# Kernel optimization log

Hardware: AMD Instinct MI355X
Metric: run time of the kernel (lower is better)

## Reference

```python
import jax, jax.numpy as jnp
import numpy as np

NUM_BINS_X = 1024
NUM_BINS_Y = 1024
XL, XH, YL, YH = 0.0, 1024.0, 0.0, 1024.0
NUM_NODES = 4_000_000
NUM_FILLER = 1_000_000
NUM_PHYS = NUM_NODES - NUM_FILLER      # physical = movable + fixed
NUM_MOVABLE = 2_500_000
UNIT_PIN_CAPACITY = 2.0                # pins per unit area capacity
PIN_STRETCH_RATIO = 1.414              # DREAMPlace default sqrt(2)
MAX_ADJ = 2.5
MIN_ADJ = 1.0 / MAX_ADJ
SPAN = 4                               # max bins any box spans per axis (sizes <= 2*bin)


def setup_inputs() -> dict:
    key = jax.random.key(0)
    k1, k2, k3, k4, k5 = jax.random.split(key, 5)
    node_size_x = 0.5 + 1.5 * jax.random.uniform(k1, (NUM_NODES,), jnp.float32)
    node_size_y = 0.5 + 1.5 * jax.random.uniform(k2, (NUM_NODES,), jnp.float32)
    pos_x = XL + jax.random.uniform(k3, (NUM_NODES,), jnp.float32) * (XH - XL - 2.0)
    pos_y = YL + jax.random.uniform(k4, (NUM_NODES,), jnp.float32) * (YH - YL - 2.0)
    pos = jnp.concatenate([pos_x, pos_y])  # [2*num_nodes], x then y
    pin_weights = jax.random.randint(k5, (NUM_PHYS,), 1, 9, jnp.int32)
    return {"pos": pos, "node_size_x": node_size_x, "node_size_y": node_size_y,
            "pin_weights": pin_weights}


def _overlap(lo, hi, bin_lo, bin_size):
    # overlap length of interval [lo,hi] with bin [bin_lo, bin_lo+bin_size]
    return jnp.clip(jnp.minimum(hi, bin_lo + bin_size) - jnp.maximum(lo, bin_lo), 0.0, None)


def reference(pos, node_size_x, node_size_y, pin_weights):
    bsx = (XH - XL) / NUM_BINS_X
    bsy = (YH - YL) / NUM_BINS_Y
    dtype = pos.dtype

    # ---- phase 1: pin density map over stretched boxes of physical nodes ----
    sx = node_size_x[:NUM_PHYS]
    sy = node_size_y[:NUM_PHYS]
    hx = 0.5 * jnp.maximum(bsx * PIN_STRETCH_RATIO, sx)  # half stretched extent
    hy = 0.5 * jnp.maximum(bsy * PIN_STRETCH_RATIO, sy)
    cx = pos[:NUM_PHYS] + 0.5 * sx
    cy = pos[NUM_NODES:NUM_NODES + NUM_PHYS] + 0.5 * sy
    xmin, xmax = cx - hx, cx + hx
    ymin, ymax = cy - hy, cy + hy
    dens = pin_weights.astype(dtype) / (4.0 * hx * hy)   # pins per unit area

    bxl = jnp.clip(jnp.floor((xmin - XL) / bsx).astype(jnp.int32), 0, NUM_BINS_X - 1)
    byl = jnp.clip(jnp.floor((ymin - YL) / bsy).astype(jnp.int32), 0, NUM_BINS_Y - 1)

    pmap = jnp.zeros(NUM_BINS_X * NUM_BINS_Y, dtype)
    for di in range(SPAN):
        bx = bxl + di
        ox = _overlap(xmin, xmax, XL + bx.astype(dtype) * bsx, bsx)
        vx = bx < NUM_BINS_X
        for dj in range(SPAN):
            by = byl + dj
            oy = _overlap(ymin, ymax, YL + by.astype(dtype) * bsy, bsy)
            v = vx & (by < NUM_BINS_Y)
            idx = jnp.where(v, bx * NUM_BINS_Y + by, 0)
            val = jnp.where(v, dens * ox * oy, 0.0)
            pmap = pmap.at[idx].add(val)

    # density -> utilization: scatter added pins*overlap/area, divide by bin area
    pmap = pmap / (bsx * bsy)
    adj = jnp.clip(pmap / UNIT_PIN_CAPACITY, MIN_ADJ, MAX_ADJ)

    # ---- phase 2: per-movable-node pin-optimized area over actual footprint ----
    mx = pos[:NUM_MOVABLE]
    my = pos[NUM_NODES:NUM_NODES + NUM_MOVABLE]
    msx = node_size_x[:NUM_MOVABLE]
    msy = node_size_y[:NUM_MOVABLE]
    bxl2 = jnp.clip(jnp.floor((mx - XL) / bsx).astype(jnp.int32), 0, NUM_BINS_X - 1)
    byl2 = jnp.clip(jnp.floor((my - YL) / bsy).astype(jnp.int32), 0, NUM_BINS_Y - 1)

    area = jnp.zeros(NUM_MOVABLE, dtype)
    for di in range(SPAN):
        bx = bxl2 + di
        ox = _overlap(mx, mx + msx, XL + bx.astype(dtype) * bsx, bsx)
        vx = bx < NUM_BINS_X
        for dj in range(SPAN):
            by = byl2 + dj
            oy = _overlap(my, my + msy, YL + by.astype(dtype) * bsy, bsy)
            v = vx & (by < NUM_BINS_Y)
            idx = jnp.where(v, bx * NUM_BINS_Y + by, 0)
            area = area + jnp.where(v, ox * oy * adj[idx], 0.0)
    return area
```

## Files before the change

### kernel.cpp

```cpp
#include <hip/hip_runtime.h>

#define NBX 1024
#define NBY 1024
#define TS 64
#define NTX (NBX / TS)
#define NTY (NBY / TS)
#define NTILES (NTX * NTY)
#define LW 66
#define LSTRIDE 67
#define CAP 13056
#define CAPM 11008

#define FB_BLOCK 512
#define FB_K 4
#define FB_CHUNK (FB_BLOCK * FB_K)

#define PMAP_SCALE 131072.0f
#define PMAP_INV   (1.0f / 131072.0f)

static constexpr int NUM_NODES   = 4000000;
static constexpr int NUM_PHYS    = 3000000;
static constexpr int NUM_MOVABLE = 2500000;
static constexpr int HALF_MOV    = NUM_MOVABLE / 2;

typedef unsigned long long u64;

static constexpr size_t OFF_PMAP  = 0;
static constexpr size_t OFF_CURS  = OFF_PMAP + (size_t)NBX * NBY * 4;
static constexpr size_t OFF_CURSM = OFF_CURS + NTILES * 4;
static constexpr size_t OFF_SLAB  = ((OFF_CURSM + NTILES * 4 + 15) / 16) * 16;
static constexpr size_t OFF_MSLAB = ((OFF_SLAB + (size_t)NTILES * CAP * 8 + 15) / 16) * 16;
static constexpr size_t WS_FULL   = OFF_MSLAB + (size_t)NTILES * CAPM * 12;

__global__ void __launch_bounds__(FB_BLOCK)
fill_both(const float* __restrict__ pos, const float* __restrict__ nsx,
          const float* __restrict__ nsy, const int* __restrict__ pw,
          unsigned* __restrict__ curs, unsigned* __restrict__ cursm,
          uint2* __restrict__ slab, uint3* __restrict__ mslab) {
    __shared__ unsigned cntp[NTILES], cntm[NTILES];
    __shared__ unsigned offp[NTILES], offm[NTILES];
    __shared__ unsigned basep[NTILES], basem[NTILES];
    __shared__ unsigned wsum[8];
    __shared__ uint2 SAB[FB_CHUNK];
    __shared__ unsigned SC[FB_CHUNK];
    __shared__ unsigned short ST[FB_CHUNK];

    const int tid = threadIdx.x;
    const int b0  = blockIdx.x * FB_CHUNK;

    if (tid < NTILES) { cntp[tid] = 0u; cntm[tid] = 0u; }
    __syncthreads();

    u64 P[FB_K];
    u64 M[FB_K];
    int TPM[FB_K];
    unsigned rkP[FB_K], rkM[FB_K];

    #pragma unroll
    for (int k = 0; k < FB_K; ++k) {
        int i = b0 + k * FB_BLOCK + tid;
        int tp = -1, tm = -1;
        if (i < NUM_PHYS) {
            float mx = pos[i], my = pos[NUM_NODES + i];
            float sx = nsx[i], sy = nsy[i];
            float hx = 0.5f * fmaxf(1.414f, sx);
            float hy = 0.5f * fmaxf(1.414f, sy);
            unsigned qhx = (unsigned)__float2int_rn((hx - 0.7f) * 1024.0f);
            unsigned qhy = (unsigned)__float2int_rn((hy - 0.7f) * 1024.0f);
            float hxd = 0.7f + (float)qhx * (1.0f / 1024.0f);
            float hyd = 0.7f + (float)qhy * (1.0f / 1024.0f);
            float xmin = mx + 0.5f * sx - hxd;
            float ymin = my + 0.5f * sy - hyd;
            int bxl = min(max((int)floorf(xmin), 0), NBX - 1);
            int byl = min(max((int)floorf(ymin), 0), NBY - 1);
            tp = (bxl >> 6) * NTY + (byl >> 6);
            int bx0 = (tp >> 4) << 6, by0 = (tp & 15) << 6;
            unsigned ex = (unsigned)__float2int_rn((xmin - (float)bx0 + 1.0f) * 8192.0f);
            unsigned ey = (unsigned)__float2int_rn((ymin - (float)by0 + 1.0f) * 8192.0f);
            P[k] = (u64)ex | ((u64)ey << 20) | ((u64)qhx << 40)
                 | ((u64)qhy << 50) | ((u64)(unsigned)(pw[i] - 1) << 60);
            rkP[k] = atomicAdd(&cntp[tp], 1u);
            if (i < NUM_MOVABLE) {
                int bxm = min(max((int)floorf(mx), 0), NBX - 1);
                int bym = min(max((int)floorf(my), 0), NBY - 1);
                tm = (bxm >> 6) * NTY + (bym >> 6);
                int bx0m = (tm >> 4) << 6, by0m = (tm & 15) << 6;
                unsigned exm = (unsigned)__float2int_rn((mx - (float)bx0m) * 8192.0f);
                unsigned eym = (unsigned)__float2int_rn((my - (float)by0m) * 8192.0f);
                unsigned qsx = (unsigned)__float2int_rn((sx - 0.5f) * 2048.0f);
                unsigned qsy = (unsigned)__float2int_rn((sy - 0.5f) * 2048.0f);
                M[k] = (u64)exm | ((u64)eym << 20) | ((u64)qsx << 40) | ((u64)qsy << 52);
                rkM[k] = atomicAdd(&cntm[tm], 1u);
            }
        }
        TPM[k] = (tp & 0xffff) | (tm << 16);
    }
    __syncthreads();

    {
        const int lane   = tid & 63;
        const int scanId = tid & 255;
        const bool isMov = tid >= 256;
        unsigned* cnt = isMov ? cntm : cntp;
        unsigned* off = isMov ? offm : offp;
        unsigned* bs  = isMov ? basem : basep;
        unsigned* gc  = isMov ? cursm : curs;

        unsigned v = cnt[scanId];
        unsigned x = v;
        #pragma unroll
        for (int d = 1; d < 64; d <<= 1) {
            unsigned y = __shfl_up(x, d);
            if (lane >= d) x += y;
        }
        if (lane == 63) wsum[tid >> 6] = x;
        __syncthreads();
        unsigned add = 0;
        const int w0  = isMov ? 4 : 0;
        const int myw = scanId >> 6;
        for (int w = 0; w < myw; ++w) add += wsum[w0 + w];
        off[scanId] = x + add - v;
        bs[scanId]  = v ? atomicAdd(&gc[scanId], v) : 0u;
    }
    __syncthreads();

    #pragma unroll
    for (int k = 0; k < FB_K; ++k) {
        int tp = (int)(short)(TPM[k] & 0xffff);
        if (tp >= 0) {
            unsigned s = offp[tp] + rkP[k];
            SAB[s] = make_uint2((unsigned)P[k], (unsigned)(P[k] >> 32));
            ST[s]  = (unsigned short)tp;
        }
    }
    __syncthreads();

    {
        unsigned totP = offp[NTILES - 1] + cntp[NTILES - 1];
        for (unsigned j = tid; j < totP; j += FB_BLOCK) {
            unsigned tile = ST[j];
            unsigned p = basep[tile] + (j - offp[tile]);
            if (p < CAP)
                slab[(size_t)tile * CAP + p] = SAB[j];
        }
    }
    __syncthreads();

    #pragma unroll
    for (int k = 0; k < FB_K; ++k) {
        int tm = TPM[k] >> 16;
        if (tm >= 0) {
            unsigned s = offm[tm] + rkM[k];
            SAB[s] = make_uint2((unsigned)M[k], (unsigned)(M[k] >> 32));
            SC[s]  = (unsigned)(b0 + k * FB_BLOCK + tid);
            ST[s]  = (unsigned short)tm;
        }
    }
    __syncthreads();

    {
        unsigned totM = offm[NTILES - 1] + cntm[NTILES - 1];
        for (unsigned j = tid; j < totM; j += FB_BLOCK) {
            unsigned tile = ST[j];
            unsigned p = basem[tile] + (j - offm[tile]);
            if (p < CAPM) {
                uint2 ab = SAB[j];
                mslab[(size_t)tile * CAPM + p] = make_uint3(ab.x, ab.y, SC[j]);
            }
        }
    }
}

__global__ void __launch_bounds__(1024)
tile_scatter(const uint2* __restrict__ slab, const unsigned* __restrict__ curs,
             float* __restrict__ pmap) {
    __shared__ unsigned lds[LW * LSTRIDE];
    int t  = blockIdx.x;
    int bx0 = (t >> 4) << 6, by0 = (t & 15) << 6;

    for (int c = threadIdx.x; c < LW * LSTRIDE; c += 1024) lds[c] = 0u;
    __syncthreads();

    unsigned n = min(curs[t], (unsigned)CAP);
    const uint2* sl = slab + (size_t)t * CAP;

    unsigned k = threadIdx.x;
    uint2 p = (k < n) ? sl[k] : make_uint2(0u, 0u);
    while (k < n) {
        unsigned kn = k + 1024;
        uint2 pn = (kn < n) ? sl[kn] : make_uint2(0u, 0u);

        u64 P = (u64)p.x | ((u64)p.y << 32);
        float xminl = (float)(P & 0xFFFFFu)         * (1.0f / 8192.0f) - 1.0f;
        float yminl = (float)((P >> 20) & 0xFFFFFu) * (1.0f / 8192.0f) - 1.0f;
        float hx = 0.7f + (float)((P >> 40) & 0x3FFu) * (1.0f / 1024.0f);
        float hy = 0.7f + (float)((P >> 50) & 0x3FFu) * (1.0f / 1024.0f);
        float pwv  = (float)(1u + (unsigned)(P >> 60));
        float dens = pwv / (4.0f * hx * hy);
        float xmaxl = xminl + 2.0f * hx;
        float ymaxl = yminl + 2.0f * hy;

        int lx0 = min(max((int)floorf(xminl), 0), TS - 1);
        int ly0 = min(max((int)floorf(yminl), 0), TS - 1);
        #pragma unroll
        for (int di = 0; di < 3; ++di) {
            float bl = (float)(lx0 + di);
            float ox = fminf(xmaxl, bl + 1.0f) - fmaxf(xminl, bl);
            if (ox <= 0.0f) continue;
            float dox = dens * ox;
            #pragma unroll
            for (int dj = 0; dj < 3; ++dj) {
                float bly = (float)(ly0 + dj);
                float oy  = fminf(ymaxl, bly + 1.0f) - fmaxf(yminl, bly);
                if (oy > 0.0f) {
                    unsigned q = (unsigned)__float2int_rn(dox * oy * PMAP_SCALE);
                    atomicAdd(&lds[(lx0 + di) * LSTRIDE + (ly0 + dj)], q);
                }
            }
        }
        p = pn;
        k = kn;
    }
    __syncthreads();

    for (int c = threadIdx.x; c < LW * LW; c += 1024) {
        int lx = c / LW, ly = c - lx * LW;
        int bx = bx0 + lx, by = by0 + ly;
        if (bx >= NBX || by >= NBY) continue;
        float v = (float)lds[lx * LSTRIDE + ly] * PMAP_INV;
        bool interior = (lx >= 2) & (lx < TS) & (ly >= 2) & (ly < TS);
        if (interior)
            pmap[bx * NBY + by] = v;
        else if (v != 0.0f)
            atomicAdd(&pmap[bx * NBY + by], v);
    }
}

__global__ void __launch_bounds__(1024)
gather_tile(const uint3* __restrict__ mslab, const unsigned* __restrict__ cursm,
            const float* __restrict__ pmap, float* __restrict__ out) {
    __shared__ float adj[LW * LSTRIDE];
    int t  = blockIdx.x;
    int bx0 = (t >> 4) << 6, by0 = (t & 15) << 6;

    for (int c = threadIdx.x; c < LW * LW; c += 1024) {
        int r = c / LW, col = c - r * LW;
        int bx = min(bx0 + r,  NBX - 1);
        int by = min(by0 + col, NBY - 1);
        adj[r * LSTRIDE + col] =
            fminf(fmaxf(pmap[bx * NBY + by] * 0.5f, 0.4f), 2.5f);
    }
    __syncthreads();

    unsigned n = min(cursm[t], (unsigned)CAPM);
    const uint3* sl = mslab + (size_t)t * CAPM;

    for (unsigned k = threadIdx.x; k < n; k += 1024) {
        uint3 p = sl[k];
        u64 M = (u64)p.x | ((u64)p.y << 32);
        float mxl = (float)(M & 0xFFFFFu)         * (1.0f / 8192.0f);
        float myl = (float)((M >> 20) & 0xFFFFFu) * (1.0f / 8192.0f);
        float sx  = 0.5f + (float)((M >> 40) & 0xFFFu) * (1.0f / 2048.0f);
        float sy  = 0.5f + (float)(M >> 52)            * (1.0f / 2048.0f);
        float xmaxl = mxl + sx;
        float ymaxl = myl + sy;

        int lx0 = min((int)mxl, TS - 1);
        int ly0 = min((int)myl, TS - 1);

        float area = 0.0f;
        #pragma unroll
        for (int di = 0; di < 3; ++di) {
            float bl = (float)(lx0 + di);
            float ox = fmaxf(fminf(xmaxl, bl + 1.0f) - fmaxf(mxl, bl), 0.0f);
            #pragma unroll
            for (int dj = 0; dj < 3; ++dj) {
                float bly = (float)(ly0 + dj);
                float oy  = fmaxf(fminf(ymaxl, bly + 1.0f) - fmaxf(myl, bly), 0.0f);
                area += ox * oy * adj[(lx0 + di) * LSTRIDE + (ly0 + dj)];
            }
        }
        out[p.z] = area;
    }
}

__global__ void __launch_bounds__(256)
scatter_pin(const float* __restrict__ pos, const float* __restrict__ nsx,
            const float* __restrict__ nsy, const int* __restrict__ pw,
            float* __restrict__ pmap) {
    int i = blockIdx.x * blockDim.x + threadIdx.x;
    if (i >= NUM_PHYS) return;
    float sx = nsx[i], sy = nsy[i];
    float hx = 0.5f * fmaxf(1.414f, sx);
    float hy = 0.5f * fmaxf(1.414f, sy);
    float cx = pos[i] + 0.5f * sx;
    float cy = pos[NUM_NODES + i] + 0.5f * sy;
    float xmin = cx - hx, xmax = cx + hx;
    float ymin = cy - hy, ymax = cy + hy;
    float dens = (float)pw[i] / (4.0f * hx * hy);
    int bxl = min(max((int)floorf(xmin), 0), NBX - 1);
    int byl = min(max((int)floorf(ymin), 0), NBY - 1);
    #pragma unroll
    for (int di = 0; di < 3; ++di) {
        float bl = (float)(bxl + di);
        float ox = fminf(xmax, bl + 1.0f) - fmaxf(xmin, bl);
        if (ox <= 0.0f) continue;
        float dox = dens * ox;
        int base = min(bxl + di, NBX - 1) * NBY;
        #pragma unroll
        for (int dj = 0; dj < 3; ++dj) {
            float bly = (float)(byl + dj);
            float oy  = fminf(ymax, bly + 1.0f) - fmaxf(ymin, bly);
            if (oy > 0.0f) atomicAdd(&pmap[base + min(byl + dj, NBY - 1)], dox * oy);
        }
    }
}

__device__ __forceinline__ float gather_one(const float* __restrict__ pos,
                                            const float* __restrict__ nsx,
                                            const float* __restrict__ nsy,
                                            const float* __restrict__ pmap,
                                            int i) {
    float mx = pos[i];
    float my = pos[NUM_NODES + i];
    float xmax = mx + nsx[i];
    float ymax = my + nsy[i];
    int bxl = min(max((int)floorf(mx), 0), NBX - 1);
    int byl = min(max((int)floorf(my), 0), NBY - 1);
    float ox[3], oy[3];
    int rowb[3], colb[3];
    #pragma unroll
    for (int d = 0; d < 3; ++d) {
        float bl  = (float)(bxl + d);
        float bly = (float)(byl + d);
        ox[d] = fmaxf(fminf(xmax, bl + 1.0f) - fmaxf(mx, bl), 0.0f);
        oy[d] = fmaxf(fminf(ymax, bly + 1.0f) - fmaxf(my, bly), 0.0f);
        rowb[d] = min(bxl + d, NBX - 1) * NBY;
        colb[d] = min(byl + d, NBY - 1);
    }
    float area = 0.0f;
    #pragma unroll
    for (int di = 0; di < 3; ++di)
        #pragma unroll
        for (int dj = 0; dj < 3; ++dj) {
            float a = fminf(fmaxf(pmap[rowb[di] + colb[dj]] * 0.5f, 0.4f), 2.5f);
            area += ox[di] * oy[dj] * a;
        }
    return area;
}

__global__ void __launch_bounds__(256)
gather_area(const float* __restrict__ pos, const float* __restrict__ nsx,
            const float* __restrict__ nsy, const float* __restrict__ pmap,
            float* __restrict__ out) {
    int i = blockIdx.x * blockDim.x + threadIdx.x;
    if (i >= HALF_MOV) return;
    int i2 = i + HALF_MOV;
    float a1 = gather_one(pos, nsx, nsy, pmap, i);
    float a2 = gather_one(pos, nsx, nsy, pmap, i2);
    out[i]  = a1;
    out[i2] = a2;
}

extern "C" void kernel_launch(void* const* d_in, const int* in_sizes, int n_in,
                              void* d_out, int out_size, void* d_ws, size_t ws_size,
                              hipStream_t stream) {
    const float* pos = (const float*)d_in[0];
    const float* nsx = (const float*)d_in[1];
    const float* nsy = (const float*)d_in[2];
    const int*   pw  = (const int*)d_in[3];
    float* out = (float*)d_out;

    char* ws = (char*)d_ws;
    float*    pmap  = (float*)(ws + OFF_PMAP);
    unsigned* curs  = (unsigned*)(ws + OFF_CURS);
    unsigned* cursm = (unsigned*)(ws + OFF_CURSM);
    uint2*    slab  = (uint2*)(ws + OFF_SLAB);
    uint3*    mslab = (uint3*)(ws + OFF_MSLAB);

    if (ws_size >= WS_FULL) {
        hipMemsetAsync(ws, 0, OFF_SLAB, stream);
        int grid = (NUM_PHYS + FB_CHUNK - 1) / FB_CHUNK;
        fill_both   <<<grid, FB_BLOCK, 0, stream>>>(pos, nsx, nsy, pw,
                                                    curs, cursm, slab, mslab);
        tile_scatter<<<NTILES, 1024, 0, stream>>>(slab, curs, pmap);
        gather_tile <<<NTILES, 1024, 0, stream>>>(mslab, cursm, pmap, out);
    } else {
        hipMemsetAsync(pmap, 0, (size_t)NBX * NBY * sizeof(float), stream);
        scatter_pin <<<(NUM_PHYS + 255) / 256, 256, 0, stream>>>(pos, nsx, nsy, pw, pmap);
        gather_area <<<(HALF_MOV + 255) / 256, 256, 0, stream>>>(pos, nsx, nsy, pmap, out);
    }
}
```

Before: 184.2 us.

## Split each tile across two blocks and double fill chunk size

Tile scatter and gather kernels now launch two blocks per tile, each handling alternating 1024-element strides of the tile's slab, so 512 blocks run instead of 256 and fill the GPU's compute units more fully. Because partial tiles now overlap, interior pmap bins are always written with atomicAdd rather than plain stores, which relies on pmap having been zeroed by the memset. The fill kernel processes 8 elements per thread instead of 4, halving the number of blocks and global cursor atomics, and precomputes base-minus-offset per tile to save an LDS read in the copy loops. The larger chunk raises shared-memory use per block and register pressure, and the extra atomics add global traffic.

Result: no change. 182.2 us (-1.1%).

```diff
diff --git a/kernel.cpp b/kernel.cpp
--- a/kernel.cpp
+++ b/kernel.cpp
@@ -12,8 +12,10 @@
 #define CAPM 11008
 
 #define FB_BLOCK 512
-#define FB_K 4
+#define FB_K 8
 #define FB_CHUNK (FB_BLOCK * FB_K)
+
+#define SPLIT 2
 
 #define PMAP_SCALE 131072.0f
 #define PMAP_INV   (1.0f / 131072.0f)
@@ -39,7 +41,7 @@
           uint2* __restrict__ slab, uint3* __restrict__ mslab) {
     __shared__ unsigned cntp[NTILES], cntm[NTILES];
     __shared__ unsigned offp[NTILES], offm[NTILES];
-    __shared__ unsigned basep[NTILES], basem[NTILES];
+    __shared__ unsigned Dp[NTILES], Dm[NTILES];
     __shared__ unsigned wsum[8];
     __shared__ uint2 SAB[FB_CHUNK];
     __shared__ unsigned SC[FB_CHUNK];
@@ -103,7 +105,7 @@
         const bool isMov = tid >= 256;
         unsigned* cnt = isMov ? cntm : cntp;
         unsigned* off = isMov ? offm : offp;
-        unsigned* bs  = isMov ? basem : basep;
+        unsigned* D   = isMov ? Dm : Dp;
         unsigned* gc  = isMov ? cursm : curs;
 
         unsigned v = cnt[scanId];
@@ -119,8 +121,10 @@
         const int w0  = isMov ? 4 : 0;
         const int myw = scanId >> 6;
         for (int w = 0; w < myw; ++w) add += wsum[w0 + w];
-        off[scanId] = x + add - v;
-        bs[scanId]  = v ? atomicAdd(&gc[scanId], v) : 0u;
+        unsigned o = x + add - v;
+        unsigned base = v ? atomicAdd(&gc[scanId], v) : 0u;
+        off[scanId] = o;
+        D[scanId]   = base - o;
     }
     __syncthreads();
 
@@ -139,7 +143,7 @@
         unsigned totP = offp[NTILES - 1] + cntp[NTILES - 1];
         for (unsigned j = tid; j < totP; j += FB_BLOCK) {
             unsigned tile = ST[j];
-            unsigned p = basep[tile] + (j - offp[tile]);
+            unsigned p = Dp[tile] + j;
             if (p < CAP)
                 slab[(size_t)tile * CAP + p] = SAB[j];
         }
@@ -162,7 +166,7 @@
         unsigned totM = offm[NTILES - 1] + cntm[NTILES - 1];
         for (unsigned j = tid; j < totM; j += FB_BLOCK) {
             unsigned tile = ST[j];
-            unsigned p = basem[tile] + (j - offm[tile]);
+            unsigned p = Dm[tile] + j;
             if (p < CAPM) {
                 uint2 ab = SAB[j];
                 mslab[(size_t)tile * CAPM + p] = make_uint3(ab.x, ab.y, SC[j]);
@@ -175,7 +179,8 @@
 tile_scatter(const uint2* __restrict__ slab, const unsigned* __restrict__ curs,
              float* __restrict__ pmap) {
     __shared__ unsigned lds[LW * LSTRIDE];
-    int t  = blockIdx.x;
+    int t   = blockIdx.x / SPLIT;
+    int sub = blockIdx.x - t * SPLIT;
     int bx0 = (t >> 4) << 6, by0 = (t & 15) << 6;
 
     for (int c = threadIdx.x; c < LW * LSTRIDE; c += 1024) lds[c] = 0u;
@@ -184,10 +189,10 @@
     unsigned n = min(curs[t], (unsigned)CAP);
     const uint2* sl = slab + (size_t)t * CAP;
 
-    unsigned k = threadIdx.x;
+    unsigned k = threadIdx.x + sub * 1024;
     uint2 p = (k < n) ? sl[k] : make_uint2(0u, 0u);
     while (k < n) {
-        unsigned kn = k + 1024;
+        unsigned kn = k + SPLIT * 1024;
         uint2 pn = (kn < n) ? sl[kn] : make_uint2(0u, 0u);
 
         u64 P = (u64)p.x | ((u64)p.y << 32);
@@ -228,10 +233,7 @@
         int bx = bx0 + lx, by = by0 + ly;
         if (bx >= NBX || by >= NBY) continue;
         float v = (float)lds[lx * LSTRIDE + ly] * PMAP_INV;
-        bool interior = (lx >= 2) & (lx < TS) & (ly >= 2) & (ly < TS);
-        if (interior)
-            pmap[bx * NBY + by] = v;
-        else if (v != 0.0f)
+        if (v != 0.0f)
             atomicAdd(&pmap[bx * NBY + by], v);
     }
 }
@@ -240,7 +242,8 @@
 gather_tile(const uint3* __restrict__ mslab, const unsigned* __restrict__ cursm,
             const float* __restrict__ pmap, float* __restrict__ out) {
     __shared__ float adj[LW * LSTRIDE];
-    int t  = blockIdx.x;
+    int t   = blockIdx.x / SPLIT;
+    int sub = blockIdx.x - t * SPLIT;
     int bx0 = (t >> 4) << 6, by0 = (t & 15) << 6;
 
     for (int c = threadIdx.x; c < LW * LW; c += 1024) {
@@ -255,7 +258,7 @@
     unsigned n = min(cursm[t], (unsigned)CAPM);
     const uint3* sl = mslab + (size_t)t * CAPM;
 
-    for (unsigned k = threadIdx.x; k < n; k += 1024) {
+    for (unsigned k = threadIdx.x + sub * 1024; k < n; k += SPLIT * 1024) {
         uint3 p = sl[k];
         u64 M = (u64)p.x | ((u64)p.y << 32);
         float mxl = (float)(M & 0xFFFFFu)         * (1.0f / 8192.0f);
@@ -383,8 +386,8 @@
         int grid = (NUM_PHYS + FB_CHUNK - 1) / FB_CHUNK;
         fill_both   <<<grid, FB_BLOCK, 0, stream>>>(pos, nsx, nsy, pw,
                                                     curs, cursm, slab, mslab);
-        tile_scatter<<<NTILES, 1024, 0, stream>>>(slab, curs, pmap);
-        gather_tile <<<NTILES, 1024, 0, stream>>>(mslab, cursm, pmap, out);
+        tile_scatter<<<NTILES * SPLIT, 1024, 0, stream>>>(slab, curs, pmap);
+        gather_tile <<<NTILES * SPLIT, 1024, 0, stream>>>(mslab, cursm, pmap, out);
     } else {
         hipMemsetAsync(pmap, 0, (size_t)NBX * NBY * sizeof(float), stream);
         scatter_pin <<<(NUM_PHYS + 255) / 256, 256, 0, stream>>>(pos, nsx, nsy, pw, pmap);
```
